# Kernel optimization log

Measured on AMD Instinct MI355X. Metric: run time of the kernel, lower is better.

## Reference

```python
import jax, jax.numpy as jnp
import numpy as np
import math

DN = ('NCHW', 'OIHW', 'NCHW')
TOTAL_STRIDE = 8.0
SCORE_OFFSET = 3.0
SCORE_SIZE = 25
BN_EPS = 1e-5


def conv2d(x, w, b, pad):
    y = jax.lax.conv_general_dilated(x, w, (1, 1), [(pad, pad), (pad, pad)],
                                     dimension_numbers=DN)
    return y + b[None, :, None, None]


def conv_module(x, w1, b1, ws, bs):
    x = conv2d(x, w1, b1, 1)
    for i in range(ws.shape[0]):
        x = conv2d(jax.nn.relu(x), ws[i], bs[i], 1)
    return x


def bn_eval(x, g, b):
    # inference-mode BatchNorm2d: running_mean=0, running_var=1
    s = g / jnp.sqrt(1.0 + BN_EPS)
    return x * s[None, :, None, None] + b[None, :, None, None]


def memory_read(fm, fq):
    B, C, T, H, W = fm.shape
    fm_flat = fm.reshape(B, C, T * H * W)          # (B, C, THW)
    fq_flat = fq.reshape(B, C, H * W)              # (B, C, HW)
    # scores: (B, THW, HW), softmax over the memory axis (THW)
    w = jnp.einsum('bct,bcq->btq', fm_flat, fq_flat) / math.sqrt(512.0)
    w = jax.nn.softmax(w, axis=1)
    mem = jnp.einsum('bct,btq->bcq', fm_flat, w).reshape(B, C, H, W)
    return jnp.concatenate([mem, fq], axis=1)      # (B, 2C, H, W)


def fm_ctr():
    gx = SCORE_OFFSET + TOTAL_STRIDE * jnp.arange(SCORE_SIZE, dtype=jnp.float32)[None, :]
    gy = SCORE_OFFSET + TOTAL_STRIDE * jnp.arange(SCORE_SIZE, dtype=jnp.float32)[:, None]
    return jnp.stack([jnp.broadcast_to(gx, (SCORE_SIZE, SCORE_SIZE)),
                      jnp.broadcast_to(gy, (SCORE_SIZE, SCORE_SIZE))], axis=-1)  # (H,W,2)


def reference(fm, fq, cls1_w, cls1_b, clsk_w, clsk_b, reg1_w, reg1_b, regk_w, regk_b,
              w_cls, b_cls, g_cls, be_cls, w_ctr, b_ctr, g_ctr, be_ctr,
              w_off, b_off, g_off, be_off, si, bi):
    y = memory_read(fm, fq)
    cls_feat = conv_module(y, cls1_w, cls1_b, clsk_w, clsk_b)
    reg_feat = conv_module(y, reg1_w, reg1_b, regk_w, regk_b)
    cls_score = bn_eval(conv2d(cls_feat, w_cls, b_cls, 0), g_cls, be_cls)  # (B,1,H,W)
    ctr_score = bn_eval(conv2d(cls_feat, w_ctr, b_ctr, 0), g_ctr, be_ctr)  # (B,1,H,W)
    offsets = bn_eval(conv2d(reg_feat, w_off, b_off, 0), g_off, be_off)    # (B,4,H,W)

    B = cls_score.shape[0]
    cls_score = cls_score.transpose(0, 2, 3, 1).reshape(B, -1, 1)
    ctr_score = ctr_score.transpose(0, 2, 3, 1).reshape(B, -1, 1)
    offsets = jnp.exp(si * offsets + bi) * TOTAL_STRIDE

    ctr = fm_ctr()                                  # (H,W,2)
    off = offsets.transpose(0, 2, 3, 1)             # (B,H,W,4)
    xy0 = ctr[None] - off[..., :2]
    xy1 = ctr[None] + off[..., 2:]
    bbox = jnp.concatenate([xy0, xy1], axis=-1).reshape(B, -1, 4)
    return cls_score, ctr_score, bbox


def setup_inputs() -> dict:
    key = jax.random.key(0)
    ks = jax.random.split(key, 16)
    B, C, T, H, W = 8, 20, 24, 25, 25
    WSC = 0.02  # small conv-weight scale to keep the 7-conv stack + exp() stable
    inp = {
        'fm': jax.random.normal(ks[0], (B, C, T, H, W), jnp.float32),
        'fq': jax.random.normal(ks[1], (B, C, H, W), jnp.float32),
        'cls1_w': jax.random.normal(ks[2], (256, 40, 3, 3), jnp.float32) * WSC,
        'cls1_b': jnp.zeros((256,), jnp.float32),
        'clsk_w': jax.random.normal(ks[3], (6, 256, 256, 3, 3), jnp.float32) * WSC,
        'clsk_b': jnp.zeros((6, 256), jnp.float32),
        'reg1_w': jax.random.normal(ks[4], (256, 40, 3, 3), jnp.float32) * WSC,
        'reg1_b': jnp.zeros((256,), jnp.float32),
        'regk_w': jax.random.normal(ks[5], (6, 256, 256, 3, 3), jnp.float32) * WSC,
        'regk_b': jnp.zeros((6, 256), jnp.float32),
        'w_cls': jax.random.normal(ks[6], (1, 256, 1, 1), jnp.float32) * WSC,
        'b_cls': jnp.zeros((1,), jnp.float32),
        'g_cls': jnp.ones((1,), jnp.float32),
        'be_cls': jnp.zeros((1,), jnp.float32),
        'w_ctr': jax.random.normal(ks[7], (1, 256, 1, 1), jnp.float32) * WSC,
        'b_ctr': jnp.zeros((1,), jnp.float32),
        'g_ctr': jnp.ones((1,), jnp.float32),
        'be_ctr': jnp.zeros((1,), jnp.float32),
        'w_off': jax.random.normal(ks[8], (4, 256, 1, 1), jnp.float32) * WSC,
        'b_off': jnp.zeros((4,), jnp.float32),
        'g_off': jnp.ones((4,), jnp.float32),
        'be_off': jnp.zeros((4,), jnp.float32),
        'si': jnp.float32(1.0),
        'bi': jnp.float32(0.0),
    }
    return inp
```

## Files before the change

kernel.cpp:

```cpp
#include <hip/hip_runtime.h>
#include <math.h>

#define BATCH 8
#define CCH 20
#define THW 15000
#define HW 625
#define SSIDE 25
#define PHW 729

#define NKEY 15000
#define TPAD 15104
#define NKT 118
#define NKC 20
#define KCHUNK 6

typedef __attribute__((ext_vector_type(8))) short bf16x8;
typedef __attribute__((ext_vector_type(4))) float f32x4;

#define YBF_OFF  0ULL
#define XA_OFF   746496ULL
#define XB_OFF   6718464ULL
#define WT0_OFF  12690432ULL
#define WT_OFF   13280256ULL
#define WTL_ELEMS 1179648ULL
#define FMT_OFF  27436032ULL
#define FM32_OFF 35169280ULL
#define FQB_OFF  42902528ULL
#define PART_OFF 43230208ULL

__device__ __forceinline__ ushort f2bf(float x) {
    unsigned u = __float_as_uint(x);
    u = (u + 0x7FFFu + ((u >> 16) & 1u)) >> 16;
    return (ushort)u;
}
__device__ __forceinline__ float bf2f(ushort v) {
    return __uint_as_float(((unsigned)v) << 16);
}

__device__ __forceinline__ void gload16(const void* g, void* l) {
    __builtin_amdgcn_global_load_lds((const __attribute__((address_space(1))) void*)g,
                                     (__attribute__((address_space(3))) void*)l, 16, 0, 0);
}

__global__ __launch_bounds__(256) void prep_fm(const float* __restrict__ fm,
                                               ushort* __restrict__ fmbT,
                                               ushort* __restrict__ fmb32) {
    __shared__ ushort sT2[256][34];
    const int tid = threadIdx.x;
    const int t0 = blockIdx.x * 256;
    const int b = blockIdx.y;
    const int t = t0 + tid;
    #pragma unroll 4
    for (int c = 0; c < CCH; c++) {
        float v = (t < NKEY) ? fm[((size_t)b * CCH + c) * THW + t] : 0.f;
        ushort h = f2bf(v);
        sT2[tid][c] = h;
        fmb32[((size_t)b * 32 + c) * TPAD + t] = h;
    }
    #pragma unroll
    for (int cz = CCH; cz < 32; cz++)
        fmb32[((size_t)b * 32 + cz) * TPAD + t] = 0;
    __syncthreads();
    const int g = tid >> 4, j = tid & 15;
    uint* dstb = (uint*)fmbT + ((size_t)b * TPAD + t0) * 16 + j;
    #pragma unroll
    for (int i = 0; i < 16; i++) {
        int r = g + 16 * i;
        uint v = 0;
        if (j < 10) v = *(const uint*)&sT2[r][2 * j];
        dstb[(size_t)r * 16] = v;
    }
}

__global__ __launch_bounds__(256) void prep_fq(const float* __restrict__ fq,
                                               ushort* __restrict__ fqb) {
    int idx = blockIdx.x * 256 + threadIdx.x;
    if (idx >= BATCH * 640) return;
    int b = idx / 640, q = idx % 640;
    const float qscale = 1.4426950408889634f * 0.04419417382415922f;
    ushort* dst = fqb + (size_t)idx * 32;
    #pragma unroll 4
    for (int c = 0; c < CCH; c++) {
        float v = (q < HW) ? fq[((size_t)b * CCH + c) * HW + q] * qscale : 0.f;
        dst[c] = f2bf(v);
    }
    #pragma unroll
    for (int c = CCH; c < 32; c++) dst[c] = 0;
}

__global__ __launch_bounds__(512) void attn_flash(const ushort* __restrict__ fmbT,
                                                  const ushort* __restrict__ fmb32,
                                                  const ushort* __restrict__ fqb,
                                                  char* __restrict__ part) {
    __shared__ __align__(16) ushort sK[2][4096];
    __shared__ __align__(16) ushort sV[2][4096];
    __shared__ __align__(16) ushort sP[8][2048];
    const int tid = threadIdx.x;
    const int wave = tid >> 6, lane = tid & 63;
    const int q16 = lane & 15, quad = lane >> 4;
    const int phys = blockIdx.x;
    const int lid = (phys & 7) * 60 + (phys >> 3);
    const int b = lid / 60;
    const int rem = lid - b * 60;
    const int kc = rem / 3;
    const int xq = rem - kc * 3;
    const int qt0 = xq * 2 + (wave >> 2);
    const bool act = (qt0 < 5);
    const int qt = act ? qt0 : 4;
    const int wq = wave & 3;

    bf16x8 Qf[2];
    #pragma unroll
    for (int nf = 0; nf < 2; nf++)
        Qf[nf] = *(const bf16x8*)(fqb + ((size_t)(b * 640 + qt * 128 + wq * 32 + nf * 16 + q16) << 5) + quad * 8);

    f32x4 O[2][2];
    #pragma unroll
    for (int nf = 0; nf < 2; nf++) { O[nf][0] = (f32x4)0.f; O[nf][1] = (f32x4)0.f; }
    float lp0 = 0.f, lp1 = 0.f;
    const f32x4 zz = (f32x4)0.f;

    const int kt0 = kc * KCHUNK;
    const int kt1 = (kt0 + KCHUNK < NKT) ? kt0 + KCHUNK : NKT;

    const int rK = tid >> 2, cK = tid & 3;
    const int rV = tid >> 4, cV = tid & 15;
    const ushort* srcK = fmbT + ((size_t)(b * TPAD + rK) << 5) + ((cK ^ (rK & 3)) << 3);
    const ushort* srcV = fmb32 + (size_t)(b * 32 + rV) * TPAD + ((cV ^ (rV & 7)) << 3);
    auto stage = [&](int kt, int bufi) {
        const int t0s = kt << 7;
        gload16(srcK + ((size_t)t0s << 5), &sK[bufi][wave << 9]);
        gload16(srcV + t0s, &sV[bufi][wave << 9]);
    };

    const int q3 = q16 & 3, q7 = q16 & 7;
    uint* const pBase = (uint*)&sP[wave][q16 << 7];

    int buf = 0;
    stage(kt0, 0);
    for (int kt = kt0; kt < kt1; kt++) {
        if (kt + 1 < kt1) {
            stage(kt + 1, buf ^ 1);
            asm volatile("s_waitcnt vmcnt(2)\n\ts_barrier" ::: "memory");
        } else {
            asm volatile("s_waitcnt vmcnt(0)\n\ts_barrier" ::: "memory");
        }
        const int t0 = kt << 7;
        const bool tail = (t0 + 128 > NKEY);

        bf16x8 Ak[8], Av[8];
        #pragma unroll
        for (int m = 0; m < 8; m++)
            Ak[m] = *(const bf16x8*)&sK[buf][((m * 16 + q16) << 5) + ((quad ^ q3) << 3)];
        #pragma unroll
        for (int mp = 0; mp < 4; mp++)
            #pragma unroll
            for (int cf = 0; cf < 2; cf++)
                Av[mp * 2 + cf] = *(const bf16x8*)&sV[buf][((cf * 16 + q16) << 7) + (((mp * 4 + quad) ^ q7) << 3)];

        f32x4 S[8][2];
        #pragma unroll
        for (int m = 0; m < 8; m++) {
            S[m][0] = __builtin_amdgcn_mfma_f32_16x16x32_bf16(Ak[m], Qf[0], zz, 0, 0, 0);
            S[m][1] = __builtin_amdgcn_mfma_f32_16x16x32_bf16(Ak[m], Qf[1], zz, 0, 0, 0);
        }

        #pragma unroll
        for (int nf = 0; nf < 2; nf++) {
            float lacc = 0.f;
            #pragma unroll
            for (int m = 0; m < 8; m++) {
                float p[4];
                #pragma unroll
                for (int i = 0; i < 4; i++) {
                    float v = __builtin_amdgcn_exp2f(S[m][nf][i]);
                    if (tail && (t0 + m * 16 + quad * 4 + i >= NKEY)) v = 0.f;
                    p[i] = v;
                }
                lacc += (p[0] + p[1]) + (p[2] + p[3]);
                uint pk0 = __builtin_amdgcn_perm(__float_as_uint(p[1]) + 0x8000u,
                                                 __float_as_uint(p[0]) + 0x8000u, 0x07060302u);
                uint pk1 = __builtin_amdgcn_perm(__float_as_uint(p[3]) + 0x8000u,
                                                 __float_as_uint(p[2]) + 0x8000u, 0x07060302u);
                uint* dst = pBase + (((m ^ q7) << 3) + quad * 2);
                dst[0] = pk0;
                dst[1] = pk1;
            }
            if (nf == 0) lp0 += lacc; else lp1 += lacc;
            #pragma unroll
            for (int mp = 0; mp < 4; mp++) {
                bf16x8 Bp = *(const bf16x8*)(pBase + ((mp * 16 + quad * 4) ^ (q7 << 3)));
                O[nf][0] = __builtin_amdgcn_mfma_f32_16x16x32_bf16(Av[mp * 2 + 0], Bp, O[nf][0], 0, 0, 0);
                O[nf][1] = __builtin_amdgcn_mfma_f32_16x16x32_bf16(Av[mp * 2 + 1], Bp, O[nf][1], 0, 0, 0);
            }
        }
        asm volatile("s_waitcnt lgkmcnt(0)\n\ts_barrier" ::: "memory");
        buf ^= 1;
    }

    lp0 += __shfl_xor(lp0, 16); lp0 += __shfl_xor(lp0, 32);
    lp1 += __shfl_xor(lp1, 16); lp1 += __shfl_xor(lp1, 32);

    if (act) {
        #pragma unroll
        for (int nf = 0; nf < 2; nf++) {
            int ql = wq * 32 + nf * 16 + q16;
            size_t rec = ((((size_t)b * 5 + qt) * NKC + kc) * 128 + ql) * 48;
            uint2 pk;
            pk.x = (unsigned)f2bf(O[nf][0][0]) | ((unsigned)f2bf(O[nf][0][1]) << 16);
            pk.y = (unsigned)f2bf(O[nf][0][2]) | ((unsigned)f2bf(O[nf][0][3]) << 16);
            *(uint2*)(part + rec + quad * 8) = pk;
            if (quad == 0) {
                uint2 pk1;
                pk1.x = (unsigned)f2bf(O[nf][1][0]) | ((unsigned)f2bf(O[nf][1][1]) << 16);
                pk1.y = (unsigned)f2bf(O[nf][1][2]) | ((unsigned)f2bf(O[nf][1][3]) << 16);
                *(uint2*)(part + rec + 32) = pk1;
                *(float*)(part + rec + 40) = (nf == 0) ? lp0 : lp1;
            }
        }
    }
}

__device__ __forceinline__ int border_pp(int bi) {
    if (bi < 27) return bi;
    if (bi < 54) return 26 * 27 + (bi - 27);
    if (bi < 79) return (bi - 53) * 27;
    return (bi - 78) * 27 + 26;
}
__global__ __launch_bounds__(256) void attn_merge_zero(const char* __restrict__ part,
                                                       const float* __restrict__ fq,
                                                       ushort* __restrict__ ybf,
                                                       ushort* __restrict__ xa,
                                                       ushort* __restrict__ xb) {
    if (blockIdx.x < 20) {
        int g = blockIdx.x * 256 + threadIdx.x;
        if (g >= BATCH * HW) return;
        int b = g / HW, q = g % HW;
        int qt = q >> 7, ql = q & 127;
        const char* pb = part + ((((size_t)b * 5 + qt) * NKC) * 128 + ql) * 48;
        float L = 0.f;
        float acc[CCH];
        #pragma unroll
        for (int c = 0; c < CCH; c++) acc[c] = 0.f;
        for (int kc = 0; kc < NKC; kc++) {
            const char* rec = pb + (size_t)kc * 128 * 48;
            L += *(const float*)(rec + 40);
            const ushort* av = (const ushort*)rec;
            #pragma unroll
            for (int c = 0; c < CCH; c++) acc[c] += bf2f(av[c]);
        }
        float inv = 1.f / L;
        int pp = (q / 25 + 1) * 27 + (q % 25) + 1;
        ushort* yb = ybf + ((size_t)b * PHW + pp) * 64;
        #pragma unroll
        for (int c = 0; c < CCH; c++) yb[c] = f2bf(acc[c] * inv);
        #pragma unroll
        for (int c = 0; c < CCH; c++) yb[20 + c] = f2bf(fq[((size_t)b * CCH + c) * HW + q]);
        #pragma unroll
        for (int c = 40; c < 64; c++) yb[c] = 0;
    } else {
        int idx = (blockIdx.x - 20) * 256 + threadIdx.x;
        ushort* buf; int cin;
        if (idx < 6656) { buf = ybf; cin = 64; }
        else if (idx < 59904) { idx -= 6656; buf = xa; cin = 256; }
        else if (idx < 113152) { idx -= 59904; buf = xb; cin = 256; }
        else return;
        int nc = cin >> 3;
        int per = 104 * nc;
        int img = idx / per, r = idx - img * per;
        int bi = r / nc, cc = r - bi * nc;
        int pp = border_pp(bi);
        uint4 z = make_uint4(0, 0, 0, 0);
        *(uint4*)&buf[((size_t)img * PHW + pp) * cin + cc * 8] = z;
    }
}

__global__ __launch_bounds__(256) void prep_weights(const float* __restrict__ cw1,
                                                    const float* __restrict__ rw1,
                                                    const float* __restrict__ cwk,
                                                    const float* __restrict__ rwk,
                                                    ushort* __restrict__ wt0,
                                                    ushort* __restrict__ wt) {
    int bid = blockIdx.x;
    if (bid < 1152) {
        int idx = bid * 256 + threadIdx.x;
        if (idx >= 2 * 9 * 256 * 64) return;
        int ic = idx & 63;
        int oc = (idx >> 6) & 255;
        int t = idx >> 14;
        int kyx = t % 9;
        int br = t / 9;
        float v = 0.f;
        if (ic < 40) {
            const float* w = br ? rw1 : cw1;
            v = w[((size_t)oc * 40 + ic) * 9 + kyx];
        }
        wt0[idx] = f2bf(v);
    } else {
        int rb = bid - 1152;
        int s = rb >> 9;
        int idx = (rb & 511) * 256 + threadIdx.x;
        if (idx >= 2 * 256 * 256) return;
        int ic = idx & 255;
        int oc = (idx >> 8) & 255;
        int br = idx >> 16;
        const float* w = br ? rwk : cwk;
        const float* src = w + (((size_t)s * 256 + oc) * 256 + ic) * 9;
        ushort* dst = wt + (size_t)s * WTL_ELEMS;
        float v[9];
        #pragma unroll
        for (int k = 0; k < 9; k++) v[k] = src[k];
        #pragma unroll
        for (int k = 0; k < 9; k++)
            dst[(((size_t)(br * 9 + k)) * 256 + oc) * 256 + ic] = f2bf(v[k]);
    }
}

__global__ __launch_bounds__(256) void conv_gemm(
    const ushort* __restrict__ xin, int cin, int in_shared, int relu_out,
    const ushort* __restrict__ wt, const float* __restrict__ bias_c,
    const float* __restrict__ bias_r, ushort* __restrict__ xout) {
    __shared__ __align__(16) ushort sA[2][4096];
    __shared__ __align__(16) ushort sBh[2][8192];
    const int tid = threadIdx.x;
    const int lane = tid & 63;
    const int wave = tid >> 6;
    const int n16 = lane & 15, quad = lane >> 4;
    const int wm = wave & 1, wn = wave >> 1;
    const int phys = blockIdx.x;
    const int lid = (phys & 7) * 80 + (phys >> 3);
    const int bb = lid / 40;
    const int rr2 = lid - bb * 40;
    const int ot = rr2 & 3, nt = rr2 >> 2;
    const int oc0 = ot * 64;
    const ushort* wbr = wt + (size_t)(bb < 8 ? 0 : 1) * 9 * 256 * cin;
    const float* bias = (bb < 8) ? bias_c : bias_r;
    const ushort* inb = xin + (size_t)(in_shared ? (bb & 7) : bb) * PHW * cin;

    const int l8 = lane >> 3, j8 = lane & 7;
    const int jj = j8 ^ l8;

    const int rA = wave * 16 + l8;
    const ushort* aS0 = wbr + (size_t)(oc0 + rA) * cin + jj * 8;
    const ushort* aS1 = aS0 + (size_t)8 * cin;
    const int segA = wave * 1024;

    const int p0 = nt * 64;
    const int ppb = p0 + 2 * (p0 / 25);
    const ushort* bS = inb + (size_t)ppb * cin + jj * 8;

    const int NCH = cin >> 6;

    auto issueA = [&](int ch, int kyx, int buf) {
        const int aoff = kyx * 256 * cin + ch * 64;
        gload16(aS0 + aoff, &sA[buf][segA]);
        gload16(aS1 + aoff, &sA[buf][segA + 512]);
    };
    auto issueB1 = [&](int ch, int q, int buf) {
        const int rb = (wave * 4 + q) * 8;
        gload16(bS + (size_t)(rb + l8) * cin + ch * 64, &sBh[buf][rb * 64]);
    };

    f32x4 acc00 = (f32x4)0.f, acc01 = (f32x4)0.f;
    f32x4 acc10 = (f32x4)0.f, acc11 = (f32x4)0.f;
    const int arow0 = wm * 32 + n16;
    const int h8 = n16 & 7;
    const int pos0 = p0 + wn * 32 + n16;
    const int pos1 = pos0 + 16;
    const int PR0 = pos0 + 28 + 2 * (pos0 / 25) - ppb;
    const int PR1 = pos1 + 28 + 2 * (pos1 / 25) - ppb;

    auto mfma_tap = [&](const ushort* sa, const ushort* sbh, int d) {
        const int row0 = PR0 + d, row1 = PR1 + d;
        const int m0 = row0 & 7, m1 = row1 & 7;
        #pragma unroll
        for (int ks = 0; ks < 2; ks++) {
            const int cq = ks * 4 + quad;
            bf16x8 a0 = *(const bf16x8*)&sa[arow0 * 64 + ((cq ^ h8) << 3)];
            bf16x8 a1 = *(const bf16x8*)&sa[(arow0 + 16) * 64 + ((cq ^ h8) << 3)];
            bf16x8 b0 = *(const bf16x8*)&sbh[row0 * 64 + ((cq ^ m0) << 3)];
            bf16x8 b1 = *(const bf16x8*)&sbh[row1 * 64 + ((cq ^ m1) << 3)];
            acc00 = __builtin_amdgcn_mfma_f32_16x16x32_bf16(a0, b0, acc00, 0, 0, 0);
            acc01 = __builtin_amdgcn_mfma_f32_16x16x32_bf16(a0, b1, acc01, 0, 0, 0);
            acc10 = __builtin_amdgcn_mfma_f32_16x16x32_bf16(a1, b0, acc10, 0, 0, 0);
            acc11 = __builtin_amdgcn_mfma_f32_16x16x32_bf16(a1, b1, acc11, 0, 0, 0);
        }
    };

    issueB1(0, 0, 0); issueB1(0, 1, 0); issueB1(0, 2, 0); issueB1(0, 3, 0);
    issueA(0, 0, 0);
    asm volatile("s_waitcnt vmcnt(0)\n\ts_barrier" ::: "memory");

    int itg = 0;
    for (int c = 0; c < NCH; c++) {
        #pragma unroll
        for (int kyx = 0; kyx < 9; kyx++, itg++) {
            if (itg + 1 < NCH * 9) {
                const int nk = (kyx == 8) ? 0 : kyx + 1;
                const int nc = (kyx == 8) ? c + 1 : c;
                issueA(nc, nk, (itg + 1) & 1);
            }
            const bool bpf = (kyx < 4) && (c + 1 < NCH);
            if (bpf) issueB1(c + 1, kyx, (c + 1) & 1);
            const int ky = kyx / 3, kx = kyx % 3;
            mfma_tap(sA[itg & 1], sBh[c & 1], (ky - 1) * 27 + (kx - 1));
            if (bpf) asm volatile("s_waitcnt vmcnt(1)\n\ts_barrier" ::: "memory");
            else     asm volatile("s_waitcnt vmcnt(0)\n\ts_barrier" ::: "memory");
        }
    }

    f32x4 accs[2][2] = {{acc00, acc01}, {acc10, acc11}};
    #pragma unroll
    for (int mf = 0; mf < 2; mf++) {
        int ocb = oc0 + wm * 32 + mf * 16 + quad * 4;
        float4 bv = *(const float4*)(bias + ocb);
        #pragma unroll
        for (int nf = 0; nf < 2; nf++) {
            int pcol = nt * 64 + wn * 32 + nf * 16 + n16;
            if (pcol >= HW) continue;
            int pp = (pcol / 25 + 1) * 27 + (pcol % 25) + 1;
            f32x4 a = accs[mf][nf];
            float v0 = a[0] + bv.x;
            float v1 = a[1] + bv.y;
            float v2 = a[2] + bv.z;
            float v3 = a[3] + bv.w;
            if (relu_out) {
                v0 = fmaxf(v0, 0.f); v1 = fmaxf(v1, 0.f);
                v2 = fmaxf(v2, 0.f); v3 = fmaxf(v3, 0.f);
            }
            uint2 st;
            st.x = (unsigned)f2bf(v0) | ((unsigned)f2bf(v1) << 16);
            st.y = (unsigned)f2bf(v2) | ((unsigned)f2bf(v3) << 16);
            *(uint2*)(&xout[((size_t)bb * PHW + pp) * 256 + ocb]) = st;
        }
    }
}

__global__ __launch_bounds__(256) void heads(const ushort* __restrict__ X,
                                             const float* __restrict__ wcls, const float* __restrict__ bcls,
                                             const float* __restrict__ gcls, const float* __restrict__ becls,
                                             const float* __restrict__ wctr, const float* __restrict__ bctr,
                                             const float* __restrict__ gctr, const float* __restrict__ bectr,
                                             const float* __restrict__ woff, const float* __restrict__ boff,
                                             const float* __restrict__ goff, const float* __restrict__ beoff,
                                             const float* __restrict__ si, const float* __restrict__ bi,
                                             float* __restrict__ out) {
    const int lane = threadIdx.x & 63, wave = threadIdx.x >> 6;
    const int gw = blockIdx.x * 4 + wave;
    const int g = gw * 16 + (lane & 15);
    const int quad = lane >> 4;
    const bool valid = (g < BATCH * HW);
    const int gc = valid ? g : (BATCH * HW - 1);
    const int b = gc / HW, p = gc % HW;
    const int pp = (p / 25 + 1) * 27 + (p % 25) + 1;
    const ushort* fc = X + ((size_t)b * PHW + pp) * 256 + quad * 64;
    const ushort* fr = X + ((size_t)(8 + b) * PHW + pp) * 256 + quad * 64;
    float ac = 0.f, at = 0.f, a0 = 0.f, a1 = 0.f, a2 = 0.f, a3 = 0.f;
    #pragma unroll
    for (int c0 = 0; c0 < 64; c0 += 8) {
        uint4 vc = *(const uint4*)(fc + c0);
        uint4 vr = *(const uint4*)(fr + c0);
        unsigned wc_[4] = {vc.x, vc.y, vc.z, vc.w};
        unsigned wr_[4] = {vr.x, vr.y, vr.z, vr.w};
        #pragma unroll
        for (int j = 0; j < 4; j++) {
            float cl = __uint_as_float(wc_[j] << 16);
            float ch = __uint_as_float(wc_[j] & 0xFFFF0000u);
            float rl = __uint_as_float(wr_[j] << 16);
            float rh = __uint_as_float(wr_[j] & 0xFFFF0000u);
            int c = quad * 64 + c0 + j * 2;
            ac += wcls[c] * cl + wcls[c + 1] * ch;
            at += wctr[c] * cl + wctr[c + 1] * ch;
            a0 += woff[c] * rl + woff[c + 1] * rh;
            a1 += woff[256 + c] * rl + woff[256 + c + 1] * rh;
            a2 += woff[512 + c] * rl + woff[512 + c + 1] * rh;
            a3 += woff[768 + c] * rl + woff[768 + c + 1] * rh;
        }
    }
    ac += __shfl_xor(ac, 16); at += __shfl_xor(at, 16);
    a0 += __shfl_xor(a0, 16); a1 += __shfl_xor(a1, 16);
    a2 += __shfl_xor(a2, 16); a3 += __shfl_xor(a3, 16);
    ac += __shfl_xor(ac, 32); at += __shfl_xor(at, 32);
    a0 += __shfl_xor(a0, 32); a1 += __shfl_xor(a1, 32);
    a2 += __shfl_xor(a2, 32); a3 += __shfl_xor(a3, 32);
    if (quad == 0 && valid) {
        const float bns = 1.f / sqrtf(1.f + 1e-5f);
        float cls = (ac + bcls[0]) * (gcls[0] * bns) + becls[0];
        float ctr = (at + bctr[0]) * (gctr[0] * bns) + bectr[0];
        float sv = si[0], bv = bi[0];
        float o0 = (a0 + boff[0]) * (goff[0] * bns) + beoff[0];
        float o1 = (a1 + boff[1]) * (goff[1] * bns) + beoff[1];
        float o2 = (a2 + boff[2]) * (goff[2] * bns) + beoff[2];
        float o3 = (a3 + boff[3]) * (goff[3] * bns) + beoff[3];
        float e0 = __expf(sv * o0 + bv) * 8.f;
        float e1 = __expf(sv * o1 + bv) * 8.f;
        float e2 = __expf(sv * o2 + bv) * 8.f;
        float e3 = __expf(sv * o3 + bv) * 8.f;
        float gx = 3.f + 8.f * (float)(p % SSIDE);
        float gy = 3.f + 8.f * (float)(p / SSIDE);
        out[g] = cls;
        out[BATCH * HW + g] = ctr;
        float* bbx = out + 2 * BATCH * HW + (size_t)g * 4;
        bbx[0] = gx - e0;
        bbx[1] = gy - e1;
        bbx[2] = gx + e2;
        bbx[3] = gy + e3;
    }
}

extern "C" void kernel_launch(void* const* d_in, const int* in_sizes, int n_in,
                              void* d_out, int out_size, void* d_ws, size_t ws_size,
                              hipStream_t stream) {
    const float* fm     = (const float*)d_in[0];
    const float* fq     = (const float*)d_in[1];
    const float* cls1_w = (const float*)d_in[2];
    const float* cls1_b = (const float*)d_in[3];
    const float* clsk_w = (const float*)d_in[4];
    const float* clsk_b = (const float*)d_in[5];
    const float* reg1_w = (const float*)d_in[6];
    const float* reg1_b = (const float*)d_in[7];
    const float* regk_w = (const float*)d_in[8];
    const float* regk_b = (const float*)d_in[9];
    const float* w_cls  = (const float*)d_in[10];
    const float* b_cls  = (const float*)d_in[11];
    const float* g_cls  = (const float*)d_in[12];
    const float* be_cls = (const float*)d_in[13];
    const float* w_ctr  = (const float*)d_in[14];
    const float* b_ctr  = (const float*)d_in[15];
    const float* g_ctr  = (const float*)d_in[16];
    const float* be_ctr = (const float*)d_in[17];
    const float* w_off  = (const float*)d_in[18];
    const float* b_off  = (const float*)d_in[19];
    const float* g_off  = (const float*)d_in[20];
    const float* be_off = (const float*)d_in[21];
    const float* si     = (const float*)d_in[22];
    const float* bi     = (const float*)d_in[23];

    char* ws = (char*)d_ws;
    ushort* YBF  = (ushort*)(ws + YBF_OFF);
    ushort* XA   = (ushort*)(ws + XA_OFF);
    ushort* XB   = (ushort*)(ws + XB_OFF);
    ushort* WT0  = (ushort*)(ws + WT0_OFF);
    ushort* WT   = (ushort*)(ws + WT_OFF);
    ushort* FMT  = (ushort*)(ws + FMT_OFF);
    ushort* FM32 = (ushort*)(ws + FM32_OFF);
    ushort* FQB  = (ushort*)(ws + FQB_OFF);
    char*   PART = ws + PART_OFF;

    prep_fm<<<dim3(59, 8), 256, 0, stream>>>(fm, FMT, FM32);
    prep_fq<<<dim3(20), 256, 0, stream>>>(fq, FQB);
    attn_flash<<<dim3(480), 512, 0, stream>>>(FMT, FM32, FQB, PART);
    attn_merge_zero<<<dim3(462), 256, 0, stream>>>(PART, fq, YBF, XA, XB);

    prep_weights<<<dim3(1152 + 512 * 6), 256, 0, stream>>>(cls1_w, reg1_w, clsk_w, regk_w, WT0, WT);

    conv_gemm<<<dim3(640), 256, 0, stream>>>(YBF, 64, 1, 1, WT0, cls1_b, reg1_b, XA);

    ushort* cur = XA;
    ushort* nxt = XB;
    for (int s = 0; s < 6; s++) {
        int relu_out = (s < 5) ? 1 : 0;
        conv_gemm<<<dim3(640), 256, 0, stream>>>(cur, 256, 0, relu_out,
            WT + (size_t)s * WTL_ELEMS,
            clsk_b + (size_t)s * 256, regk_b + (size_t)s * 256, nxt);
        ushort* tmp = cur; cur = nxt; nxt = tmp;
    }

    heads<<<dim3(79), 256, 0, stream>>>(cur, w_cls, b_cls, g_cls, be_cls,
                                        w_ctr, b_ctr, g_ctr, be_ctr,
                                        w_off, b_off, g_off, be_off, si, bi,
                                        (float*)d_out);
}
```

Baseline: 346.9 us.

## Merge prep kernels, restructure attention barriers, pad P tile, add MFMA priority

```diff
diff --git a/kernel.cpp b/kernel.cpp
--- a/kernel.cpp
+++ b/kernel.cpp
@@ -42,50 +42,52 @@
                                      (__attribute__((address_space(3))) void*)l, 16, 0, 0);
 }
 
-__global__ __launch_bounds__(256) void prep_fm(const float* __restrict__ fm,
-                                               ushort* __restrict__ fmbT,
-                                               ushort* __restrict__ fmb32) {
+__global__ __launch_bounds__(256) void prep_fmq(const float* __restrict__ fm,
+                                                const float* __restrict__ fq,
+                                                ushort* __restrict__ fmbT,
+                                                ushort* __restrict__ fmb32,
+                                                ushort* __restrict__ fqb) {
     __shared__ ushort sT2[256][34];
+    const int bid = blockIdx.x;
     const int tid = threadIdx.x;
-    const int t0 = blockIdx.x * 256;
-    const int b = blockIdx.y;
-    const int t = t0 + tid;
-    #pragma unroll 4
-    for (int c = 0; c < CCH; c++) {
-        float v = (t < NKEY) ? fm[((size_t)b * CCH + c) * THW + t] : 0.f;
-        ushort h = f2bf(v);
-        sT2[tid][c] = h;
-        fmb32[((size_t)b * 32 + c) * TPAD + t] = h;
-    }
-    #pragma unroll
-    for (int cz = CCH; cz < 32; cz++)
-        fmb32[((size_t)b * 32 + cz) * TPAD + t] = 0;
-    __syncthreads();
-    const int g = tid >> 4, j = tid & 15;
-    uint* dstb = (uint*)fmbT + ((size_t)b * TPAD + t0) * 16 + j;
-    #pragma unroll
-    for (int i = 0; i < 16; i++) {
-        int r = g + 16 * i;
-        uint v = 0;
-        if (j < 10) v = *(const uint*)&sT2[r][2 * j];
-        dstb[(size_t)r * 16] = v;
-    }
-}
-
-__global__ __launch_bounds__(256) void prep_fq(const float* __restrict__ fq,
-                                               ushort* __restrict__ fqb) {
-    int idx = blockIdx.x * 256 + threadIdx.x;
-    if (idx >= BATCH * 640) return;
-    int b = idx / 640, q = idx % 640;
-    const float qscale = 1.4426950408889634f * 0.04419417382415922f;
-    ushort* dst = fqb + (size_t)idx * 32;
-    #pragma unroll 4
-    for (int c = 0; c < CCH; c++) {
-        float v = (q < HW) ? fq[((size_t)b * CCH + c) * HW + q] * qscale : 0.f;
-        dst[c] = f2bf(v);
-    }
-    #pragma unroll
-    for (int c = CCH; c < 32; c++) dst[c] = 0;
+    if (bid < 472) {
+        const int t0 = (bid % 59) * 256;
+        const int b = bid / 59;
+        const int t = t0 + tid;
+        #pragma unroll 4
+        for (int c = 0; c < CCH; c++) {
+            float v = (t < NKEY) ? fm[((size_t)b * CCH + c) * THW + t] : 0.f;
+            ushort h = f2bf(v);
+            sT2[tid][c] = h;
+            fmb32[((size_t)b * 32 + c) * TPAD + t] = h;
+        }
+        #pragma unroll
+        for (int cz = CCH; cz < 32; cz++)
+            fmb32[((size_t)b * 32 + cz) * TPAD + t] = 0;
+        __syncthreads();
+        const int g = tid >> 4, j = tid & 15;
+        uint* dstb = (uint*)fmbT + ((size_t)b * TPAD + t0) * 16 + j;
+        #pragma unroll
+        for (int i = 0; i < 16; i++) {
+            int r = g + 16 * i;
+            uint v = 0;
+            if (j < 10) v = *(const uint*)&sT2[r][2 * j];
+            dstb[(size_t)r * 16] = v;
+        }
+    } else {
+        int idx = (bid - 472) * 256 + tid;
+        if (idx >= BATCH * 640) return;
+        int b = idx / 640, q = idx % 640;
+        const float qscale = 1.4426950408889634f * 0.04419417382415922f;
+        ushort* dst = fqb + (size_t)idx * 32;
+        #pragma unroll 4
+        for (int c = 0; c < CCH; c++) {
+            float v = (q < HW) ? fq[((size_t)b * CCH + c) * HW + q] * qscale : 0.f;
+            dst[c] = f2bf(v);
+        }
+        #pragma unroll
+        for (int c = CCH; c < 32; c++) dst[c] = 0;
+    }
 }
 
 __global__ __launch_bounds__(512) void attn_flash(const ushort* __restrict__ fmbT,
@@ -94,7 +96,7 @@
                                                   char* __restrict__ part) {
     __shared__ __align__(16) ushort sK[2][4096];
     __shared__ __align__(16) ushort sV[2][4096];
-    __shared__ __align__(16) ushort sP[8][2048];
+    __shared__ __align__(16) ushort sP[8][16][136];
     const int tid = threadIdx.x;
     const int wave = tid >> 6, lane = tid & 63;
     const int q16 = lane & 15, quad = lane >> 4;
@@ -134,17 +136,14 @@
     };
 
     const int q3 = q16 & 3, q7 = q16 & 7;
-    uint* const pBase = (uint*)&sP[wave][q16 << 7];
+    uint* const pBase = (uint*)&sP[wave][q16][0];
 
     int buf = 0;
     stage(kt0, 0);
+    asm volatile("s_waitcnt vmcnt(0)\n\ts_barrier" ::: "memory");
     for (int kt = kt0; kt < kt1; kt++) {
-        if (kt + 1 < kt1) {
-            stage(kt + 1, buf ^ 1);
-            asm volatile("s_waitcnt vmcnt(2)\n\ts_barrier" ::: "memory");
-        } else {
-            asm volatile("s_waitcnt vmcnt(0)\n\ts_barrier" ::: "memory");
-        }
+        const bool nl = (kt + 1 < kt1);
+        if (nl) stage(kt + 1, buf ^ 1);
         const int t0 = kt << 7;
         const bool tail = (t0 + 128 > NKEY);
 
@@ -159,11 +158,13 @@
                 Av[mp * 2 + cf] = *(const bf16x8*)&sV[buf][((cf * 16 + q16) << 7) + (((mp * 4 + quad) ^ q7) << 3)];
 
         f32x4 S[8][2];
+        __builtin_amdgcn_s_setprio(1);
         #pragma unroll
         for (int m = 0; m < 8; m++) {
             S[m][0] = __builtin_amdgcn_mfma_f32_16x16x32_bf16(Ak[m], Qf[0], zz, 0, 0, 0);
             S[m][1] = __builtin_amdgcn_mfma_f32_16x16x32_bf16(Ak[m], Qf[1], zz, 0, 0, 0);
         }
+        __builtin_amdgcn_s_setprio(0);
 
         #pragma unroll
         for (int nf = 0; nf < 2; nf++) {
@@ -182,19 +183,21 @@
                                                  __float_as_uint(p[0]) + 0x8000u, 0x07060302u);
                 uint pk1 = __builtin_amdgcn_perm(__float_as_uint(p[3]) + 0x8000u,
                                                  __float_as_uint(p[2]) + 0x8000u, 0x07060302u);
-                uint* dst = pBase + (((m ^ q7) << 3) + quad * 2);
+                uint* dst = pBase + m * 8 + quad * 2;
                 dst[0] = pk0;
                 dst[1] = pk1;
             }
             if (nf == 0) lp0 += lacc; else lp1 += lacc;
+            __builtin_amdgcn_s_setprio(1);
             #pragma unroll
             for (int mp = 0; mp < 4; mp++) {
-                bf16x8 Bp = *(const bf16x8*)(pBase + ((mp * 16 + quad * 4) ^ (q7 << 3)));
+                bf16x8 Bp = *(const bf16x8*)&sP[wave][q16][mp * 32 + quad * 8];
                 O[nf][0] = __builtin_amdgcn_mfma_f32_16x16x32_bf16(Av[mp * 2 + 0], Bp, O[nf][0], 0, 0, 0);
                 O[nf][1] = __builtin_amdgcn_mfma_f32_16x16x32_bf16(Av[mp * 2 + 1], Bp, O[nf][1], 0, 0, 0);
             }
-        }
-        asm volatile("s_waitcnt lgkmcnt(0)\n\ts_barrier" ::: "memory");
+            __builtin_amdgcn_s_setprio(0);
+        }
+        if (nl) asm volatile("s_waitcnt vmcnt(0) lgkmcnt(0)\n\ts_barrier" ::: "memory");
         buf ^= 1;
     }
 
@@ -547,8 +550,7 @@
     ushort* FQB  = (ushort*)(ws + FQB_OFF);
     char*   PART = ws + PART_OFF;
 
-    prep_fm<<<dim3(59, 8), 256, 0, stream>>>(fm, FMT, FM32);
-    prep_fq<<<dim3(20), 256, 0, stream>>>(fq, FQB);
+    prep_fmq<<<dim3(492), 256, 0, stream>>>(fm, fq, FMT, FM32, FQB);
     attn_flash<<<dim3(480), 512, 0, stream>>>(FMT, FM32, FQB, PART);
     attn_merge_zero<<<dim3(462), 256, 0, stream>>>(PART, fq, YBF, XA, XB);
 
```

Measured after the change: 334.1 us. 1.04x faster.
